# Optimization experiments

Measured on AMD Instinct MI355X. Metric: run time of the kernel, lower is better.

## Reference

```python
import jax, jax.numpy as jnp
import numpy as np

TEM = 0.5
BN_EPS = 1e-5
ROWS, IN_FEA, OUT_FEA = 16384, 512, 128


def setup_inputs() -> dict:
    key = jax.random.key(0)
    ks = jax.random.split(key, 3)
    doc_fea = jax.random.normal(ks[0], (ROWS, IN_FEA), dtype=jnp.float32)
    W1 = jax.random.normal(ks[1], (IN_FEA, OUT_FEA), dtype=jnp.float32) * 0.02
    b1 = jnp.zeros((OUT_FEA,), dtype=jnp.float32)
    gamma = jnp.ones((OUT_FEA,), dtype=jnp.float32)
    beta = jnp.zeros((OUT_FEA,), dtype=jnp.float32)
    W2 = jax.random.normal(ks[2], (OUT_FEA, OUT_FEA), dtype=jnp.float32) * 0.02
    b2 = jnp.zeros((OUT_FEA,), dtype=jnp.float32)
    return {"doc_fea": doc_fea, "W1": W1, "b1": b1, "gamma": gamma,
            "beta": beta, "W2": W2, "b2": b2}


def _l2_normalize(x):
    # matches torch F.normalize(dim=1, eps=1e-12)
    n = jnp.linalg.norm(x, axis=1, keepdims=True)
    return x / jnp.maximum(n, 1e-12)


def _half_loss(a, b):
    # rows of a, b are unit-norm, so cosine sim == matmul
    between = jnp.exp(a @ b.T / TEM)          # [N, N]
    refl = jnp.exp(a @ a.T / TEM)             # [N, N]
    pos = jnp.diagonal(between)
    denom = refl.sum(axis=1) + between.sum(axis=1) - jnp.diagonal(refl)
    return -jnp.log(pos / denom)


def reference(doc_fea, W1, b1, gamma, beta, W2, b2):
    # projector: Linear -> BatchNorm1d (training stats) -> ReLU -> Linear
    h = doc_fea @ W1 + b1
    mu = h.mean(axis=0)
    var = h.var(axis=0)  # biased variance, as used by torch BN normalization
    h = (h - mu) * jax.lax.rsqrt(var + BN_EPS) * gamma + beta
    h = jax.nn.relu(h)
    out = h @ W2 + b2
    out = _l2_normalize(out)
    # original: out_1 = out[indices where i%2!=0], out_2 = out[i%2==0]
    out_1 = out[1::2]
    out_2 = out[0::2]
    l1 = _half_loss(out_1, out_2)
    l2 = _half_loss(out_2, out_1)
    loss = (l1 + l2) * 0.5
    return loss.mean()
```

## Files before the change

### kernel.cpp

```cpp
#include <hip/hip_runtime.h>

typedef __attribute__((ext_vector_type(8))) short short8;
typedef __attribute__((ext_vector_type(4))) float f32x4;

typedef const __attribute__((address_space(1))) unsigned int as1_u32;
typedef __attribute__((address_space(3))) unsigned int as3_u32;

#define E2f   7.38905609893065f
#define OSCALE 1.69864357f

#if __has_builtin(__builtin_amdgcn_exp2f)
#define EXP2(x) __builtin_amdgcn_exp2f(x)
#else
#define EXP2(x) exp2f(x)
#endif

__device__ inline unsigned short f2bf(float f){
    union { float f; unsigned int u; } x; x.f = f;
    unsigned int u = x.u;
    return (unsigned short)((u + 0x7fffu + ((u >> 16) & 1u)) >> 16);
}

__device__ inline short8 pack8(float4 a, float4 b){
    short8 t;
    t[0]=(short)f2bf(a.x); t[1]=(short)f2bf(a.y); t[2]=(short)f2bf(a.z); t[3]=(short)f2bf(a.w);
    t[4]=(short)f2bf(b.x); t[5]=(short)f2bf(b.y); t[6]=(short)f2bf(b.z); t[7]=(short)f2bf(b.w);
    return t;
}

__global__ __launch_bounds__(256) void k_prep(const float* __restrict__ W1, const float* __restrict__ W2,
                                              short* __restrict__ W1T, short* __restrict__ W2T){
    int idx = blockIdx.x*256 + threadIdx.x;
    if(idx < 512*128){
        int n = idx >> 9, k = idx & 511;
        W1T[idx] = (short)f2bf(W1[k*128 + n]);
    } else {
        int i2 = idx - 512*128;
        int n = i2 >> 7, k = i2 & 127;
        W2T[i2] = (short)f2bf(W2[k*128 + n]);
    }
}

__global__ __launch_bounds__(256) void k_gemm1(const float* __restrict__ doc, const float* __restrict__ b1,
                                               const short* __restrict__ W1T, float* __restrict__ h,
                                               float* __restrict__ bsum, float* __restrict__ bsq){
    int bid = blockIdx.x;
    int tid = threadIdx.x;
    int w = tid >> 6, l = tid & 63, lr = l & 15, lk = l >> 4;
    int rowA = bid*64 + w*16 + lr;

    short8 a[16];
    const float* dp = doc + rowA*512 + lk*8;
    #pragma unroll
    for(int c=0;c<16;c++){
        float4 f0 = *(const float4*)(dp + c*32);
        float4 f1 = *(const float4*)(dp + c*32 + 4);
        a[c] = pack8(f0, f1);
    }

    f32x4 acc[8];
    #pragma unroll
    for(int ct=0; ct<8; ct++) acc[ct] = (f32x4){0.f,0.f,0.f,0.f};

    const short* wb = W1T + lr*512 + lk*8;
    #pragma unroll
    for(int c=0;c<16;c++){
        #pragma unroll
        for(int ct=0; ct<8; ct++){
            short8 b = *(const short8*)(wb + ct*16*512 + c*32);
            acc[ct] = __builtin_amdgcn_mfma_f32_16x16x32_bf16(a[c], b, acc[ct], 0,0,0);
        }
    }

    __shared__ float lds_s[4][128];
    __shared__ float lds_q[4][128];
    int rowD = bid*64 + w*16 + lk*4;
    #pragma unroll
    for(int ct=0; ct<8; ct++){
        float bb = b1[ct*16 + lr];
        float s = 0.f, q = 0.f;
        #pragma unroll
        for(int r=0;r<4;r++){
            float v = acc[ct][r] + bb;
            h[(rowD + r)*128 + ct*16 + lr] = v;
            s += v; q += v*v;
        }
        s += __shfl_xor(s,16); s += __shfl_xor(s,32);
        q += __shfl_xor(q,16); q += __shfl_xor(q,32);
        if(lk==0){ lds_s[w][ct*16+lr] = s; lds_q[w][ct*16+lr] = q; }
    }
    __syncthreads();
    if(tid < 128){
        float S = lds_s[0][tid]+lds_s[1][tid]+lds_s[2][tid]+lds_s[3][tid];
        float Q = lds_q[0][tid]+lds_q[1][tid]+lds_q[2][tid]+lds_q[3][tid];
        bsum[bid*128 + tid] = S;
        bsq [bid*128 + tid] = Q;
    }
}

__global__ __launch_bounds__(128) void k_bnfin(const float* __restrict__ bsum, const float* __restrict__ bsq,
                                               const float* __restrict__ gamma, const float* __restrict__ beta,
                                               float* __restrict__ bnA, float* __restrict__ bnB){
    int c = threadIdx.x;
    float S=0.f, Q=0.f;
    for(int b=0;b<256;b++){ S += bsum[b*128+c]; Q += bsq[b*128+c]; }
    float mu = S * (1.0f/16384.0f);
    float var = Q * (1.0f/16384.0f) - mu*mu;
    float A = gamma[c] * rsqrtf(var + 1e-5f);
    bnA[c] = A;
    bnB[c] = beta[c] - mu*A;
}

__global__ __launch_bounds__(256) void k_gemm2(const float* __restrict__ h, const short* __restrict__ W2T,
                                               const float* __restrict__ bnA, const float* __restrict__ bnB,
                                               const float* __restrict__ b2,
                                               short* __restrict__ o1s, short* __restrict__ o2s,
                                               float* __restrict__ dvec){
    int bid = blockIdx.x;
    int tid = threadIdx.x;
    int w = tid >> 6, l = tid & 63, lr = l & 15, lk = l >> 4;
    int rowA = bid*64 + w*16 + lr;

    short8 a[4];
    const float* hp = h + rowA*128 + lk*8;
    #pragma unroll
    for(int c=0;c<4;c++){
        float4 h0 = *(const float4*)(hp + c*32);
        float4 h1 = *(const float4*)(hp + c*32 + 4);
        float4 A0 = *(const float4*)(bnA + c*32 + lk*8);
        float4 A1 = *(const float4*)(bnA + c*32 + lk*8 + 4);
        float4 B0 = *(const float4*)(bnB + c*32 + lk*8);
        float4 B1 = *(const float4*)(bnB + c*32 + lk*8 + 4);
        float4 v0, v1;
        v0.x = fmaxf(h0.x*A0.x + B0.x, 0.f); v0.y = fmaxf(h0.y*A0.y + B0.y, 0.f);
        v0.z = fmaxf(h0.z*A0.z + B0.z, 0.f); v0.w = fmaxf(h0.w*A0.w + B0.w, 0.f);
        v1.x = fmaxf(h1.x*A1.x + B1.x, 0.f); v1.y = fmaxf(h1.y*A1.y + B1.y, 0.f);
        v1.z = fmaxf(h1.z*A1.z + B1.z, 0.f); v1.w = fmaxf(h1.w*A1.w + B1.w, 0.f);
        a[c] = pack8(v0, v1);
    }

    f32x4 acc[8];
    #pragma unroll
    for(int ct=0; ct<8; ct++) acc[ct] = (f32x4){0.f,0.f,0.f,0.f};
    const short* wb = W2T + lr*128 + lk*8;
    #pragma unroll
    for(int c=0;c<4;c++){
        #pragma unroll
        for(int ct=0; ct<8; ct++){
            short8 b = *(const short8*)(wb + ct*16*128 + c*32);
            acc[ct] = __builtin_amdgcn_mfma_f32_16x16x32_bf16(a[c], b, acc[ct], 0,0,0);
        }
    }

    #pragma unroll
    for(int ct=0; ct<8; ct++){
        float bb = b2[ct*16 + lr];
        #pragma unroll
        for(int r=0;r<4;r++) acc[ct][r] += bb;
    }
    float n2[4] = {0.f,0.f,0.f,0.f};
    #pragma unroll
    for(int ct=0; ct<8; ct++){
        #pragma unroll
        for(int r=0;r<4;r++) n2[r] += acc[ct][r]*acc[ct][r];
    }
    #pragma unroll
    for(int r=0;r<4;r++){
        n2[r] += __shfl_xor(n2[r],1); n2[r] += __shfl_xor(n2[r],2);
        n2[r] += __shfl_xor(n2[r],4); n2[r] += __shfl_xor(n2[r],8);
    }
    float sc[4];
    #pragma unroll
    for(int r=0;r<4;r++) sc[r] = 1.0f / fmaxf(sqrtf(n2[r]), 1e-12f);
    #pragma unroll
    for(int ct=0; ct<8; ct++){
        #pragma unroll
        for(int r=0;r<4;r++) acc[ct][r] *= sc[r];
    }
    float dp0 = 0.f, dp1 = 0.f;
    #pragma unroll
    for(int ct=0; ct<8; ct++){
        dp0 += acc[ct][0]*acc[ct][1];
        dp1 += acc[ct][2]*acc[ct][3];
    }
    dp0 += __shfl_xor(dp0,1); dp0 += __shfl_xor(dp0,2); dp0 += __shfl_xor(dp0,4); dp0 += __shfl_xor(dp0,8);
    dp1 += __shfl_xor(dp1,1); dp1 += __shfl_xor(dp1,2); dp1 += __shfl_xor(dp1,4); dp1 += __shfl_xor(dp1,8);
    int r0 = bid*64 + w*16 + lk*4;
    if(lr==0){
        dvec[(r0>>1)    ] = dp0;
        dvec[(r0>>1) + 1] = dp1;
    }
    #pragma unroll
    for(int ct=0; ct<8; ct++){
        #pragma unroll
        for(int r=0;r<4;r++){
            int grow = r0 + r;
            int col  = ct*16 + lr;
            short bits = (short)f2bf(acc[ct][r] * OSCALE);
            if(grow & 1) o1s[(grow>>1)*128 + col] = bits;
            else         o2s[(grow>>1)*128 + col] = bits;
        }
    }
}

__global__ __launch_bounds__(256) void k_sim(const short* __restrict__ o1s, const short* __restrict__ o2s,
                                             float* __restrict__ r11p, float* __restrict__ r22p,
                                             float* __restrict__ r12p, float* __restrict__ c12p){
    int bx = blockIdx.x, by = blockIdx.y, pz = blockIdx.z;
    const short* A = (pz==1) ? o2s : o1s;
    const short* B = (pz==0) ? o1s : o2s;
    float* rowp = (pz==0) ? r11p : (pz==1 ? r22p : r12p);
    const bool colsum = (pz==2);

    int tid = threadIdx.x;
    int w = tid>>6, l = tid&63, lr = l&15, lk = l>>4;

    __shared__ __align__(16) short lds[2][8192];
    __shared__ float cs_lds[2][4][64];

    short8 a[2][4];
    {
        const short* ap = A + (bx*128 + w*32 + lr)*128 + lk*8;
        #pragma unroll
        for(int rt=0;rt<2;rt++)
            #pragma unroll
            for(int c=0;c<4;c++)
                a[rt][c] = *(const short8*)(ap + rt*2048 + c*32);
    }

    int sb[4];
    #pragma unroll
    for(int c=0;c<4;c++) sb[c] = lr*256 + ((((c*4+lk) ^ (lr&7)))<<4);

    const short* gsrc[4];
    #pragma unroll
    for(int i=0;i<4;i++){
        int chunk = i*4 + w;
        int row = chunk*4 + (l>>4);
        int col16 = (l&15) ^ (row&7);
        gsrc[i] = B + (by*512 + row)*128 + col16*8;
    }

    #pragma unroll
    for(int i=0;i<4;i++){
        __builtin_amdgcn_global_load_lds((as1_u32*)gsrc[i],
            (as3_u32*)(&lds[0][(i*4+w)*512]), 16, 0, 0);
        gsrc[i] += 8192;
    }
    asm volatile("s_waitcnt vmcnt(0)" ::: "memory");
    __syncthreads();

    float rs[2][4] = {{0.f,0.f,0.f,0.f},{0.f,0.f,0.f,0.f}};
    int buf = 0;
    const char* lbase = (const char*)&lds[0][0];

    for(int t=0;t<8;t++){
        if(t<7){
            #pragma unroll
            for(int i=0;i<4;i++){
                __builtin_amdgcn_global_load_lds((as1_u32*)gsrc[i],
                    (as3_u32*)(&lds[buf^1][(i*4+w)*512]), 16, 0, 0);
                gsrc[i] += 8192;
            }
        }
        const char* lb = lbase + buf*16384;
        #pragma unroll
        for(int jt=0;jt<4;jt++){
            short8 b0 = *(const short8*)(lb + jt*4096 + sb[0]);
            short8 b1 = *(const short8*)(lb + jt*4096 + sb[1]);
            short8 b2 = *(const short8*)(lb + jt*4096 + sb[2]);
            short8 b3 = *(const short8*)(lb + jt*4096 + sb[3]);
            f32x4 c0 = (f32x4){0.f,0.f,0.f,0.f};
            f32x4 c1 = (f32x4){0.f,0.f,0.f,0.f};
            c0 = __builtin_amdgcn_mfma_f32_16x16x32_bf16(a[0][0], b0, c0,0,0,0);
            c1 = __builtin_amdgcn_mfma_f32_16x16x32_bf16(a[1][0], b0, c1,0,0,0);
            c0 = __builtin_amdgcn_mfma_f32_16x16x32_bf16(a[0][1], b1, c0,0,0,0);
            c1 = __builtin_amdgcn_mfma_f32_16x16x32_bf16(a[1][1], b1, c1,0,0,0);
            c0 = __builtin_amdgcn_mfma_f32_16x16x32_bf16(a[0][2], b2, c0,0,0,0);
            c1 = __builtin_amdgcn_mfma_f32_16x16x32_bf16(a[1][2], b2, c1,0,0,0);
            c0 = __builtin_amdgcn_mfma_f32_16x16x32_bf16(a[0][3], b3, c0,0,0,0);
            c1 = __builtin_amdgcn_mfma_f32_16x16x32_bf16(a[1][3], b3, c1,0,0,0);
            float e00 = EXP2(c0[0]), e01 = EXP2(c0[1]), e02 = EXP2(c0[2]), e03 = EXP2(c0[3]);
            float e10 = EXP2(c1[0]), e11 = EXP2(c1[1]), e12 = EXP2(c1[2]), e13 = EXP2(c1[3]);
            rs[0][0]+=e00; rs[0][1]+=e01; rs[0][2]+=e02; rs[0][3]+=e03;
            rs[1][0]+=e10; rs[1][1]+=e11; rs[1][2]+=e12; rs[1][3]+=e13;
            if(colsum){
                float cv = ((e00+e01)+(e02+e03)) + ((e10+e11)+(e12+e13));
                cv += __shfl_xor(cv,16); cv += __shfl_xor(cv,32);
                if(lk==0) cs_lds[t&1][w][jt*16+lr] = cv;
            }
        }
        asm volatile("s_waitcnt vmcnt(0)" ::: "memory");
        __syncthreads();
        if(colsum && tid < 64){
            float v = cs_lds[t&1][0][tid]+cs_lds[t&1][1][tid]
                    + cs_lds[t&1][2][tid]+cs_lds[t&1][3][tid];
            c12p[bx*8192 + by*512 + t*64 + tid] = v;
        }
        buf ^= 1;
    }

    #pragma unroll
    for(int rt=0;rt<2;rt++){
        #pragma unroll
        for(int r=0;r<4;r++){
            rs[rt][r] += __shfl_xor(rs[rt][r],1);
            rs[rt][r] += __shfl_xor(rs[rt][r],2);
            rs[rt][r] += __shfl_xor(rs[rt][r],4);
            rs[rt][r] += __shfl_xor(rs[rt][r],8);
        }
        if(lr==0){
            float4 v; v.x=rs[rt][0]; v.y=rs[rt][1]; v.z=rs[rt][2]; v.w=rs[rt][3];
            *(float4*)(rowp + by*8192 + bx*128 + w*32 + rt*16 + lk*4) = v;
        }
    }
}

__global__ __launch_bounds__(256) void k_loss1(const float* __restrict__ r11, const float* __restrict__ r12,
                                               const float* __restrict__ r22, const float* __restrict__ c12,
                                               const float* __restrict__ dvec, float* __restrict__ lpart){
    int i = blockIdx.x*256 + threadIdx.x;
    float s11=0.f, s12=0.f, s22=0.f, s21=0.f;
    #pragma unroll
    for(int s=0;s<16;s++){
        s11 += r11[s*8192+i]; s12 += r12[s*8192+i]; s22 += r22[s*8192+i];
    }
    #pragma unroll
    for(int s=0;s<64;s++) s21 += c12[s*8192+i];
    float d1 = s11 - E2f + s12;
    float d2 = s22 - E2f + s21;
    float loss = 0.5f*(logf(d1)+logf(d2)) - 2.0f*dvec[i];
    loss += __shfl_xor(loss,1);  loss += __shfl_xor(loss,2);  loss += __shfl_xor(loss,4);
    loss += __shfl_xor(loss,8);  loss += __shfl_xor(loss,16); loss += __shfl_xor(loss,32);
    __shared__ float lds[4];
    if((threadIdx.x & 63) == 0) lds[threadIdx.x >> 6] = loss;
    __syncthreads();
    if(threadIdx.x == 0) lpart[blockIdx.x] = lds[0]+lds[1]+lds[2]+lds[3];
}

__global__ __launch_bounds__(64) void k_loss2(const float* __restrict__ lpart, float* __restrict__ out){
    if(threadIdx.x == 0){
        float s = 0.f;
        for(int i=0;i<32;i++) s += lpart[i];
        out[0] = s * (1.0f/8192.0f);
    }
}

extern "C" void kernel_launch(void* const* d_in, const int* in_sizes, int n_in,
                              void* d_out, int out_size, void* d_ws, size_t ws_size,
                              hipStream_t stream){
    (void)in_sizes; (void)n_in; (void)out_size; (void)ws_size;
    const float* doc   = (const float*)d_in[0];
    const float* W1    = (const float*)d_in[1];
    const float* b1    = (const float*)d_in[2];
    const float* gamma = (const float*)d_in[3];
    const float* beta  = (const float*)d_in[4];
    const float* W2    = (const float*)d_in[5];
    const float* b2    = (const float*)d_in[6];
    float* out = (float*)d_out;

    char* ws = (char*)d_ws;
    float* h     = (float*)(ws + 0);
    float* c12p  = (float*)(ws + 0);
    float* r11p  = (float*)(ws + 2097152);
    float* r22p  = (float*)(ws + 2621440);
    float* r12p  = (float*)(ws + 3145728);
    short* W1T   = (short*)(ws + 8388608);
    short* W2T   = (short*)(ws + 8519680);
    short* o1s   = (short*)(ws + 8552448);
    short* o2s   = (short*)(ws + 10649600);
    float* dvec  = (float*)(ws + 12746752);
    float* bnA   = (float*)(ws + 12779520);
    float* bnB   = (float*)(ws + 12780032);
    float* bsum  = (float*)(ws + 12780544);
    float* bsq   = (float*)(ws + 12911616);
    float* lpart = (float*)(ws + 13042688);

    k_prep <<<320, 256, 0, stream>>>(W1, W2, W1T, W2T);
    k_gemm1<<<256, 256, 0, stream>>>(doc, b1, W1T, h, bsum, bsq);
    k_bnfin<<<1, 128, 0, stream>>>(bsum, bsq, gamma, beta, bnA, bnB);
    k_gemm2<<<256, 256, 0, stream>>>(h, W2T, bnA, bnB, b2, o1s, o2s, dvec);
    dim3 sg(64, 16, 3);
    k_sim  <<<sg, 256, 0, stream>>>(o1s, o2s, r11p, r22p, r12p, c12p);
    k_loss1<<<32, 256, 0, stream>>>(r11p, r12p, r22p, c12p, dvec, lpart);
    k_loss2<<<1, 64, 0, stream>>>(lpart, out);
}
```

Before: 129.1 us.

## Exploit symmetry of self-similarity blocks to compute only upper triangle

Result: slower. 217.2 us (+68.2%).

```diff
diff --git a/kernel.cpp b/kernel.cpp
--- a/kernel.cpp
+++ b/kernel.cpp
@@ -9,11 +9,7 @@
 #define E2f   7.38905609893065f
 #define OSCALE 1.69864357f
 
-#if __has_builtin(__builtin_amdgcn_exp2f)
-#define EXP2(x) __builtin_amdgcn_exp2f(x)
-#else
 #define EXP2(x) exp2f(x)
-#endif
 
 __device__ inline unsigned short f2bf(float f){
     union { float f; unsigned int u; } x; x.f = f;
@@ -205,18 +201,31 @@
 
 __global__ __launch_bounds__(256) void k_sim(const short* __restrict__ o1s, const short* __restrict__ o2s,
                                              float* __restrict__ r11p, float* __restrict__ r22p,
-                                             float* __restrict__ r12p, float* __restrict__ c12p){
-    int bx = blockIdx.x, by = blockIdx.y, pz = blockIdx.z;
+                                             float* __restrict__ r12p, float* __restrict__ c11p,
+                                             float* __restrict__ c22p, float* __restrict__ c12p){
+    int bid = blockIdx.x;
+    int pz, bx, by;
+    if(bid < 1024){
+        pz = 2; bx = bid & 63; by = bid >> 6;
+    } else {
+        int t = bid - 1024;
+        pz = (t >= 544) ? 1 : 0;
+        int rem = (t >= 544) ? t - 544 : t;
+        int bq = 0;
+        while(rem >= 4*(16-bq)){ rem -= 4*(16-bq); bq++; }
+        bx = 4*bq + (rem & 3);
+        by = bq + (rem >> 2);
+    }
     const short* A = (pz==1) ? o2s : o1s;
     const short* B = (pz==0) ? o1s : o2s;
     float* rowp = (pz==0) ? r11p : (pz==1 ? r22p : r12p);
-    const bool colsum = (pz==2);
+    float* colp = (pz==0) ? c11p : (pz==1 ? c22p : c12p);
+    const bool do_col = (pz==2) || (by > (bx>>2));
 
     int tid = threadIdx.x;
     int w = tid>>6, l = tid&63, lr = l&15, lk = l>>4;
 
     __shared__ __align__(16) short lds[2][8192];
-    __shared__ float cs_lds[2][4][64];
 
     short8 a[2][4];
     {
@@ -235,8 +244,7 @@
     const short* gsrc[4];
     #pragma unroll
     for(int i=0;i<4;i++){
-        int chunk = i*4 + w;
-        int row = chunk*4 + (l>>4);
+        int row = (i*4 + w)*4 + (l>>4);
         int col16 = (l&15) ^ (row&7);
         gsrc[i] = B + (by*512 + row)*128 + col16*8;
     }
@@ -251,10 +259,12 @@
     __syncthreads();
 
     float rs[2][4] = {{0.f,0.f,0.f,0.f},{0.f,0.f,0.f,0.f}};
-    int buf = 0;
+    float cs8[8];
     const char* lbase = (const char*)&lds[0][0];
 
+    #pragma unroll
     for(int t=0;t<8;t++){
+        const int buf = t & 1;
         if(t<7){
             #pragma unroll
             for(int i=0;i<4;i++){
@@ -264,6 +274,7 @@
             }
         }
         const char* lb = lbase + buf*16384;
+        float cst = 0.f;
         #pragma unroll
         for(int jt=0;jt<4;jt++){
             short8 b0 = *(const short8*)(lb + jt*4096 + sb[0]);
@@ -284,20 +295,15 @@
             float e10 = EXP2(c1[0]), e11 = EXP2(c1[1]), e12 = EXP2(c1[2]), e13 = EXP2(c1[3]);
             rs[0][0]+=e00; rs[0][1]+=e01; rs[0][2]+=e02; rs[0][3]+=e03;
             rs[1][0]+=e10; rs[1][1]+=e11; rs[1][2]+=e12; rs[1][3]+=e13;
-            if(colsum){
+            if(do_col){
                 float cv = ((e00+e01)+(e02+e03)) + ((e10+e11)+(e12+e13));
                 cv += __shfl_xor(cv,16); cv += __shfl_xor(cv,32);
-                if(lk==0) cs_lds[t&1][w][jt*16+lr] = cv;
+                if(jt == lk) cst = cv;
             }
         }
+        cs8[t] = cst;
         asm volatile("s_waitcnt vmcnt(0)" ::: "memory");
         __syncthreads();
-        if(colsum && tid < 64){
-            float v = cs_lds[t&1][0][tid]+cs_lds[t&1][1][tid]
-                    + cs_lds[t&1][2][tid]+cs_lds[t&1][3][tid];
-            c12p[bx*8192 + by*512 + t*64 + tid] = v;
-        }
-        buf ^= 1;
     }
 
     #pragma unroll
@@ -314,17 +320,31 @@
             *(float4*)(rowp + by*8192 + bx*128 + w*32 + rt*16 + lk*4) = v;
         }
     }
-}
-
-__global__ __launch_bounds__(256) void k_loss1(const float* __restrict__ r11, const float* __restrict__ r12,
-                                               const float* __restrict__ r22, const float* __restrict__ c12,
+
+    if(do_col){
+        float* lf = (float*)&lds[0][0];
+        #pragma unroll
+        for(int t=0;t<8;t++) lf[w*512 + t*64 + l] = cs8[t];
+        __syncthreads();
+        int j0 = tid, j1 = tid + 256;
+        float v0 = lf[j0] + lf[512+j0] + lf[1024+j0] + lf[1536+j0];
+        float v1 = lf[j1] + lf[512+j1] + lf[1024+j1] + lf[1536+j1];
+        colp[bx*8192 + by*512 + j0] = v0;
+        colp[bx*8192 + by*512 + j1] = v1;
+    }
+}
+
+__global__ __launch_bounds__(256) void k_loss1(const float* __restrict__ r11, const float* __restrict__ r22,
+                                               const float* __restrict__ r12, const float* __restrict__ c11,
+                                               const float* __restrict__ c22, const float* __restrict__ c12,
                                                const float* __restrict__ dvec, float* __restrict__ lpart){
     int i = blockIdx.x*256 + threadIdx.x;
-    float s11=0.f, s12=0.f, s22=0.f, s21=0.f;
-    #pragma unroll
-    for(int s=0;s<16;s++){
-        s11 += r11[s*8192+i]; s12 += r12[s*8192+i]; s22 += r22[s*8192+i];
-    }
+    int byi = i >> 9;
+    float s11=0.f, s22=0.f, s12=0.f, s21=0.f;
+    for(int by=byi; by<16; by++){ s11 += r11[by*8192+i]; s22 += r22[by*8192+i]; }
+    for(int bx=0; bx<4*byi; bx++){ s11 += c11[bx*8192+i]; s22 += c22[bx*8192+i]; }
+    #pragma unroll
+    for(int s=0;s<16;s++) s12 += r12[s*8192+i];
     #pragma unroll
     for(int s=0;s<64;s++) s21 += c12[s*8192+i];
     float d1 = s11 - E2f + s12;
@@ -361,10 +381,12 @@
 
     char* ws = (char*)d_ws;
     float* h     = (float*)(ws + 0);
-    float* c12p  = (float*)(ws + 0);
-    float* r11p  = (float*)(ws + 2097152);
-    float* r22p  = (float*)(ws + 2621440);
-    float* r12p  = (float*)(ws + 3145728);
+    float* c11p  = (float*)(ws + 0);
+    float* c22p  = (float*)(ws + 2097152);
+    float* c12p  = (float*)(ws + 4194304);
+    float* r11p  = (float*)(ws + 6291456);
+    float* r22p  = (float*)(ws + 6815744);
+    float* r12p  = (float*)(ws + 7340032);
     short* W1T   = (short*)(ws + 8388608);
     short* W2T   = (short*)(ws + 8519680);
     short* o1s   = (short*)(ws + 8552448);
@@ -380,8 +402,7 @@
     k_gemm1<<<256, 256, 0, stream>>>(doc, b1, W1T, h, bsum, bsq);
     k_bnfin<<<1, 128, 0, stream>>>(bsum, bsq, gamma, beta, bnA, bnB);
     k_gemm2<<<256, 256, 0, stream>>>(h, W2T, bnA, bnB, b2, o1s, o2s, dvec);
-    dim3 sg(64, 16, 3);
-    k_sim  <<<sg, 256, 0, stream>>>(o1s, o2s, r11p, r22p, r12p, c12p);
-    k_loss1<<<32, 256, 0, stream>>>(r11p, r12p, r22p, c12p, dvec, lpart);
+    k_sim  <<<2112, 256, 0, stream>>>(o1s, o2s, r11p, r22p, r12p, c11p, c22p, c12p);
+    k_loss1<<<32, 256, 0, stream>>>(r11p, r22p, r12p, c11p, c22p, c12p, dvec, lpart);
     k_loss2<<<1, 64, 0, stream>>>(lpart, out);
 }
```

## Compute reverse cross-similarity row sums with a fourth grid slice instead of column sums

Applied to the files above, without the earlier changes.

Result: slower. 154.0 us (+19.3%).

```diff
diff --git a/kernel.cpp b/kernel.cpp
--- a/kernel.cpp
+++ b/kernel.cpp
@@ -9,11 +9,7 @@
 #define E2f   7.38905609893065f
 #define OSCALE 1.69864357f
 
-#if __has_builtin(__builtin_amdgcn_exp2f)
-#define EXP2(x) __builtin_amdgcn_exp2f(x)
-#else
 #define EXP2(x) exp2f(x)
-#endif
 
 __device__ inline unsigned short f2bf(float f){
     union { float f; unsigned int u; } x; x.f = f;
@@ -205,18 +201,16 @@
 
 __global__ __launch_bounds__(256) void k_sim(const short* __restrict__ o1s, const short* __restrict__ o2s,
                                              float* __restrict__ r11p, float* __restrict__ r22p,
-                                             float* __restrict__ r12p, float* __restrict__ c12p){
+                                             float* __restrict__ r12p, float* __restrict__ r21p){
     int bx = blockIdx.x, by = blockIdx.y, pz = blockIdx.z;
-    const short* A = (pz==1) ? o2s : o1s;
-    const short* B = (pz==0) ? o1s : o2s;
-    float* rowp = (pz==0) ? r11p : (pz==1 ? r22p : r12p);
-    const bool colsum = (pz==2);
+    const short* A = (pz & 1) ? o2s : o1s;
+    const short* B = (pz==1 || pz==2) ? o2s : o1s;
+    float* rowp = (pz==0) ? r11p : (pz==1 ? r22p : (pz==2 ? r12p : r21p));
 
     int tid = threadIdx.x;
     int w = tid>>6, l = tid&63, lr = l&15, lk = l>>4;
 
     __shared__ __align__(16) short lds[2][8192];
-    __shared__ float cs_lds[2][4][64];
 
     short8 a[2][4];
     {
@@ -280,23 +274,13 @@
             c1 = __builtin_amdgcn_mfma_f32_16x16x32_bf16(a[1][2], b2, c1,0,0,0);
             c0 = __builtin_amdgcn_mfma_f32_16x16x32_bf16(a[0][3], b3, c0,0,0,0);
             c1 = __builtin_amdgcn_mfma_f32_16x16x32_bf16(a[1][3], b3, c1,0,0,0);
-            float e00 = EXP2(c0[0]), e01 = EXP2(c0[1]), e02 = EXP2(c0[2]), e03 = EXP2(c0[3]);
-            float e10 = EXP2(c1[0]), e11 = EXP2(c1[1]), e12 = EXP2(c1[2]), e13 = EXP2(c1[3]);
-            rs[0][0]+=e00; rs[0][1]+=e01; rs[0][2]+=e02; rs[0][3]+=e03;
-            rs[1][0]+=e10; rs[1][1]+=e11; rs[1][2]+=e12; rs[1][3]+=e13;
-            if(colsum){
-                float cv = ((e00+e01)+(e02+e03)) + ((e10+e11)+(e12+e13));
-                cv += __shfl_xor(cv,16); cv += __shfl_xor(cv,32);
-                if(lk==0) cs_lds[t&1][w][jt*16+lr] = cv;
-            }
+            rs[0][0] += EXP2(c0[0]); rs[0][1] += EXP2(c0[1]);
+            rs[0][2] += EXP2(c0[2]); rs[0][3] += EXP2(c0[3]);
+            rs[1][0] += EXP2(c1[0]); rs[1][1] += EXP2(c1[1]);
+            rs[1][2] += EXP2(c1[2]); rs[1][3] += EXP2(c1[3]);
         }
         asm volatile("s_waitcnt vmcnt(0)" ::: "memory");
         __syncthreads();
-        if(colsum && tid < 64){
-            float v = cs_lds[t&1][0][tid]+cs_lds[t&1][1][tid]
-                    + cs_lds[t&1][2][tid]+cs_lds[t&1][3][tid];
-            c12p[bx*8192 + by*512 + t*64 + tid] = v;
-        }
         buf ^= 1;
     }
 
@@ -316,17 +300,16 @@
     }
 }
 
-__global__ __launch_bounds__(256) void k_loss1(const float* __restrict__ r11, const float* __restrict__ r12,
-                                               const float* __restrict__ r22, const float* __restrict__ c12,
+__global__ __launch_bounds__(256) void k_loss1(const float* __restrict__ r11, const float* __restrict__ r22,
+                                               const float* __restrict__ r12, const float* __restrict__ r21,
                                                const float* __restrict__ dvec, float* __restrict__ lpart){
     int i = blockIdx.x*256 + threadIdx.x;
-    float s11=0.f, s12=0.f, s22=0.f, s21=0.f;
+    float s11=0.f, s22=0.f, s12=0.f, s21=0.f;
     #pragma unroll
     for(int s=0;s<16;s++){
-        s11 += r11[s*8192+i]; s12 += r12[s*8192+i]; s22 += r22[s*8192+i];
-    }
-    #pragma unroll
-    for(int s=0;s<64;s++) s21 += c12[s*8192+i];
+        s11 += r11[s*8192+i]; s22 += r22[s*8192+i];
+        s12 += r12[s*8192+i]; s21 += r21[s*8192+i];
+    }
     float d1 = s11 - E2f + s12;
     float d2 = s22 - E2f + s21;
     float loss = 0.5f*(logf(d1)+logf(d2)) - 2.0f*dvec[i];
@@ -361,10 +344,10 @@
 
     char* ws = (char*)d_ws;
     float* h     = (float*)(ws + 0);
-    float* c12p  = (float*)(ws + 0);
-    float* r11p  = (float*)(ws + 2097152);
-    float* r22p  = (float*)(ws + 2621440);
-    float* r12p  = (float*)(ws + 3145728);
+    float* r11p  = (float*)(ws + 0);
+    float* r22p  = (float*)(ws + 524288);
+    float* r12p  = (float*)(ws + 1048576);
+    float* r21p  = (float*)(ws + 1572864);
     short* W1T   = (short*)(ws + 8388608);
     short* W2T   = (short*)(ws + 8519680);
     short* o1s   = (short*)(ws + 8552448);
@@ -380,8 +363,8 @@
     k_gemm1<<<256, 256, 0, stream>>>(doc, b1, W1T, h, bsum, bsq);
     k_bnfin<<<1, 128, 0, stream>>>(bsum, bsq, gamma, beta, bnA, bnB);
     k_gemm2<<<256, 256, 0, stream>>>(h, W2T, bnA, bnB, b2, o1s, o2s, dvec);
-    dim3 sg(64, 16, 3);
-    k_sim  <<<sg, 256, 0, stream>>>(o1s, o2s, r11p, r22p, r12p, c12p);
-    k_loss1<<<32, 256, 0, stream>>>(r11p, r12p, r22p, c12p, dvec, lpart);
+    dim3 sg(64, 16, 4);
+    k_sim  <<<sg, 256, 0, stream>>>(o1s, o2s, r11p, r22p, r12p, r21p);
+    k_loss1<<<32, 256, 0, stream>>>(r11p, r22p, r12p, r21p, dvec, lpart);
     k_loss2<<<1, 64, 0, stream>>>(lpart, out);
 }
```
